# Performance work log

Measured on AMD Instinct MI355X. Metric: run time of the kernel, lower is better.

## Reference

```python
import jax, jax.numpy as jnp
import numpy as np

N_ITERS = 100   # fixed ADMM (OSQP-style) iteration count
RHO = 1.0       # ADMM penalty
SIGMA = 1e-6    # OSQP regularization


def setup_inputs() -> dict:
    key = jax.random.key(0)
    ks = jax.random.split(key, 12)
    B, S, H, nA = 16384, 512, 1024, 24
    mEq, mIneq = 4, 8
    state = jax.random.normal(ks[0], (B, S), dtype=jnp.float32)
    Aeq = jax.random.normal(ks[1], (mEq, nA), dtype=jnp.float32)
    beq = jax.random.normal(ks[2], (mEq,), dtype=jnp.float32)
    A = jax.random.normal(ks[3], (mIneq, nA), dtype=jnp.float32)
    b = jax.random.uniform(ks[4], (mIneq,), dtype=jnp.float32)
    ub = jnp.ones((nA,), dtype=jnp.float32)
    lb = jnp.zeros((nA,), dtype=jnp.float32)
    # MLP parameters (3 Dense layers as in the flax module)
    W1 = jax.random.normal(ks[5], (S, H), dtype=jnp.float32) / np.sqrt(S).astype(np.float32)
    b1 = jnp.zeros((H,), dtype=jnp.float32)
    W2 = jax.random.normal(ks[6], (H, H), dtype=jnp.float32) / np.sqrt(H).astype(np.float32)
    b2 = jnp.zeros((H,), dtype=jnp.float32)
    W3 = jax.random.normal(ks[7], (H, nA), dtype=jnp.float32) / np.sqrt(H).astype(np.float32)
    b3 = jnp.zeros((nA,), dtype=jnp.float32)
    return dict(state=state, Aeq=Aeq, beq=beq, A=A, b=b, ub=ub, lb=lb,
                W1=W1, b1=b1, W2=W2, b2=b2, W3=W3, b3=b3)


def reference(state, Aeq, beq, A, b, ub, lb, W1, b1, W2, b2, W3, b3):
    # ---- 3-layer MLP ----
    h = jax.nn.relu(state @ W1 + b1)
    h = jax.nn.relu(h @ W2 + b2)
    raw = h @ W3 + b3                      # [B, n]
    n = raw.shape[-1]
    I = jnp.eye(n, dtype=raw.dtype)
    # ---- stack constraints exactly as solve_qp: [Aeq; A_ineq; I; -I] ----
    A_tot = jnp.concatenate([Aeq, A, I, -I], axis=0)            # [M, n]
    neg_inf = jnp.full((A.shape[0],), -jnp.inf, dtype=raw.dtype)
    l_tot = jnp.concatenate([beq, neg_inf, lb, -ub])            # [M]
    u_tot = jnp.concatenate([beq, b, ub, -lb])                  # [M]
    # ---- OSQP-style ADMM: min 0.5||x||^2 - raw'x  s.t. l <= A_tot x <= u ----
    q = -raw                                                    # [B, n]
    M = (1.0 + SIGMA) * I + RHO * (A_tot.T @ A_tot)             # [n, n] (P = I)
    Minv = jnp.linalg.inv(M)
    B_, m = q.shape[0], A_tot.shape[0]
    X0 = jnp.zeros_like(q)
    Z0 = jnp.zeros((B_, m), dtype=q.dtype)
    Y0 = jnp.zeros((B_, m), dtype=q.dtype)

    def step(carry, _):
        X, Z, Y = carry
        rhs = SIGMA * X - q + (RHO * Z - Y) @ A_tot             # [B, n]
        Xn = rhs @ Minv.T                                       # [B, n]
        Zt = Xn @ A_tot.T                                       # [B, m]
        Zn = jnp.clip(Zt + Y / RHO, l_tot, u_tot)
        Yn = Y + RHO * (Zt - Zn)
        return (Xn, Zn, Yn), None

    (X, Z, Y), _ = jax.lax.scan(step, (X0, Z0, Y0), None, length=N_ITERS)
    return X
```

## Files before the change

kernel.cpp:

```cpp
#include <hip/hip_runtime.h>

using uint = unsigned int;
using ushort = unsigned short;

typedef __attribute__((ext_vector_type(8))) short bf16x8;
typedef __attribute__((ext_vector_type(4))) short bf16x4;
typedef __attribute__((ext_vector_type(4))) float f32x4;

#define ADMM_ITERS 100
#define RHO_C 1.0f
#define SIGMA_C 1e-6f

__device__ inline ushort f2bf(float f) {
  union { float f; uint u; } c; c.f = f;
  uint u = c.u;
  uint r = (u + 0x7fffu + ((u >> 16) & 1u)) >> 16;
  return (ushort)r;
}

__device__ inline void gload_lds16(const void* g, void* l) {
  __builtin_amdgcn_global_load_lds(
      (const __attribute__((address_space(1))) void*)g,
      (__attribute__((address_space(3))) void*)l, 16, 0, 0);
}

__device__ inline void splitPack(const float* x, bf16x8& hi, bf16x8& lo) {
#pragma unroll
  for (int j = 0; j < 8; ++j) {
    uint b = __float_as_uint(x[j]);
    uint hb = b & 0xffff0000u;
    float lf = x[j] - __uint_as_float(hb);
    hi[j] = (short)(b >> 16);
    lo[j] = (short)(__float_as_uint(lf) >> 16);
  }
}

__device__ inline void splitPack4(const f32x4& x, bf16x4& hi, bf16x4& lo) {
  uint b0 = __float_as_uint(x[0]), b1 = __float_as_uint(x[1]);
  uint b2 = __float_as_uint(x[2]), b3 = __float_as_uint(x[3]);
  float l0 = x[0] - __uint_as_float(b0 & 0xffff0000u);
  float l1 = x[1] - __uint_as_float(b1 & 0xffff0000u);
  float l2 = x[2] - __uint_as_float(b2 & 0xffff0000u);
  float l3 = x[3] - __uint_as_float(b3 & 0xffff0000u);
  union { uint u[2]; bf16x4 v; } ch, cl;
  ch.u[0] = __builtin_amdgcn_perm(b1, b0, 0x07060302u);
  ch.u[1] = __builtin_amdgcn_perm(b3, b2, 0x07060302u);
  cl.u[0] = __builtin_amdgcn_perm(__float_as_uint(l1), __float_as_uint(l0), 0x07060302u);
  cl.u[1] = __builtin_amdgcn_perm(__float_as_uint(l3), __float_as_uint(l2), 0x07060302u);
  hi = ch.v; lo = cl.v;
}

__device__ void transpose_body(const float* __restrict__ in, ushort* __restrict__ out,
                               int R, int C, int Cout, int bx, int by, int tid) {
  __shared__ float t[32][33];
  const int c0 = bx * 32, r0 = by * 32;
  const int tx = tid & 31, ty = tid >> 5;
  for (int rr = ty; rr < 32; rr += 8) {
    int r = r0 + rr, c = c0 + tx;
    float v = 0.0f;
    if (r < R && c < C) v = in[(long)r * C + c];
    t[rr][tx] = v;
  }
  __syncthreads();
  for (int rr = ty; rr < 32; rr += 8) {
    int c = c0 + rr, r = r0 + tx;
    if (c < Cout && r < R) out[(long)c * R + r] = f2bf(t[tx][rr]);
  }
}

__device__ void setup_body(const float* __restrict__ Aeq, const float* __restrict__ beq,
                           const float* __restrict__ A, const float* __restrict__ b,
                           const float* __restrict__ ub, const float* __restrict__ lb,
                           ushort* __restrict__ Th, ushort* __restrict__ Tl,
                           ushort* __restrict__ T0h, ushort* __restrict__ T0l,
                           float* __restrict__ blp, float* __restrict__ bup, int t) {
  __shared__ float Aug[24][48];
  __shared__ float A12[12 * 24];
  __shared__ float fac[24];
  __shared__ float Tx[24][36];
  for (int i = t; i < 48 * 64; i += 256) { Th[i] = 0; Tl[i] = 0; }
  for (int i = t; i < 48 * 32; i += 256) { T0h[i] = 0; T0l[i] = 0; }
  if (t < 96)  A12[t] = Aeq[t];
  if (t < 192) A12[96 + t] = A[t];
  __syncthreads();
  for (int idx = t; idx < 576; idx += 256) {
    int j = idx / 24, k = idx % 24;
    float s = (j == k) ? (1.0f + SIGMA_C + 2.0f * RHO_C) : 0.0f;
    for (int r = 0; r < 12; ++r) s += RHO_C * A12[r * 24 + j] * A12[r * 24 + k];
    Aug[j][k] = s;
    Aug[j][24 + k] = (j == k) ? 1.0f : 0.0f;
  }
  __syncthreads();
  for (int p = 0; p < 24; ++p) {
    float rp = 1.0f / Aug[p][p];
    if (t < 24) fac[t] = Aug[t][p];
    __syncthreads();
    if (t < 48) Aug[p][t] *= rp;
    __syncthreads();
    for (int idx = t; idx < 24 * 48; idx += 256) {
      int r = idx / 48, c = idx % 48;
      if (r != p) Aug[r][c] -= fac[r] * Aug[p][c];
    }
    __syncthreads();
  }
  auto splitStore = [](ushort* hp, ushort* lp, int i, float v) {
    ushort hs = f2bf(v);
    float hf = __uint_as_float(((uint)hs) << 16);
    ushort ls = f2bf(v - hf);
    hp[i] = hs; lp[i] = ls;
  };
  for (int idx = t; idx < 24 * 36; idx += 256) {
    int n = idx / 36, k = idx % 36;
    float v;
    if (k < 24) v = 2.0f * Aug[n][24 + k];
    else {
      v = 0.0f;
      for (int j = 0; j < 24; ++j) v += Aug[n][24 + j] * A12[(k - 24) * 24 + j];
    }
    Tx[n][k] = v;
    splitStore(Th, Tl, n * 64 + k, v);
  }
  __syncthreads();
  for (int idx = t; idx < 12 * 36; idx += 256) {
    int m = idx / 36, k = idx % 36;
    float v = 0.0f;
    for (int j = 0; j < 24; ++j) v += A12[m * 24 + j] * Tx[j][k];
    splitStore(Th, Tl, (24 + m) * 64 + k, v);
  }
  for (int idx = t; idx < 36 * 24; idx += 256) {
    int n = idx / 24, k = idx % 24;
    float v;
    if (n < 24) v = Aug[n][24 + k];
    else {
      v = 0.0f;
      for (int j = 0; j < 24; ++j) v += A12[(n - 24) * 24 + j] * Aug[j][24 + k];
    }
    splitStore(T0h, T0l, n * 32 + k, v);
  }
  if (t < 48) {
    float lv, uv;
    if (t < 24)      { lv = lb[t]; uv = ub[t]; }
    else if (t < 28) { lv = beq[t - 24]; uv = lv; }
    else if (t < 36) { lv = -1e30f; uv = b[t - 28]; }
    else             { lv = -1e30f; uv = 1e30f; }
    blp[t] = lv; bup[t] = uv;
  }
}

__global__ void prep_all(
    const float* __restrict__ state, ushort* __restrict__ stateB, int n4,
    const float* __restrict__ W1, ushort* __restrict__ W1T,
    const float* __restrict__ W2, ushort* __restrict__ W2T,
    const float* __restrict__ W3, ushort* __restrict__ W3T,
    const float* __restrict__ Aeq, const float* __restrict__ beq,
    const float* __restrict__ A, const float* __restrict__ b,
    const float* __restrict__ ub, const float* __restrict__ lb,
    ushort* __restrict__ Th, ushort* __restrict__ Tl,
    ushort* __restrict__ T0h, ushort* __restrict__ T0l,
    float* __restrict__ blp, float* __restrict__ bup) {
  const int nConv = n4 >> 8;
  int bb = blockIdx.x;
  if (bb < nConv) {
    int i = bb * 256 + threadIdx.x;
    if (i < n4) {
      float4 v = ((const float4*)state)[i];
      uint2 p;
      p.x = (uint)f2bf(v.x) | ((uint)f2bf(v.y) << 16);
      p.y = (uint)f2bf(v.z) | ((uint)f2bf(v.w) << 16);
      ((uint2*)stateB)[i] = p;
    }
    return;
  }
  bb -= nConv;
  if (bb < 512)  { transpose_body(W1, W1T, 512, 1024, 1024, bb & 31, bb >> 5, threadIdx.x); return; }
  bb -= 512;
  if (bb < 1024) { transpose_body(W2, W2T, 1024, 1024, 1024, bb & 31, bb >> 5, threadIdx.x); return; }
  bb -= 1024;
  if (bb < 32)   { transpose_body(W3, W3T, 1024, 24, 32, 0, bb, threadIdx.x); return; }
  setup_body(Aeq, beq, A, b, ub, lb, Th, Tl, T0h, T0l, blp, bup, threadIdx.x);
}

template<int BM, int BN, int WM, int WN, int TM, int TN, int MODE>
__global__ __launch_bounds__(256) void gemm_bt(
    const ushort* __restrict__ A, const ushort* __restrict__ Bt,
    const float* __restrict__ bias, void* __restrict__ Cout_,
    int K, int ldc, int nvalid) {
  __shared__ char lds[(BM + BN) * 64];
  char* ldsA = lds;
  char* ldsB = lds + BM * 64;

  const int tid = threadIdx.x;
  const int wave = tid >> 6;
  const int lane = tid & 63;
  const int blockM = blockIdx.y * BM;
  const int blockN = blockIdx.x * BN;
  const int wm = (wave / WN) * (TM * 16);
  const int wn = (wave % WN) * (TN * 16);

  f32x4 acc[TM][TN] = {};

  const int l15 = lane & 15;
  const int kq = lane >> 4;
  constexpr int AI = BM / 16;
  constexpr int TOT = (BM + BN) / 16;
  const int srow = lane >> 2;
  const int kb = (lane & 3) ^ ((srow >> 1) & 3);

  for (int k0 = 0; k0 < K; k0 += 32) {
    for (int inst = wave; inst < TOT; inst += 4) {
      const bool isA = inst < AI;
      const int i = isA ? inst : inst - AI;
      const ushort* gp = (isA ? A : Bt)
          + (long)((isA ? blockM : blockN) + i * 16 + srow) * K + (k0 + kb * 8);
      char* lp = (isA ? ldsA : ldsB) + i * 1024;
      gload_lds16(gp, lp);
    }
    __syncthreads();

    bf16x8 af[TM], bfr[TN];
#pragma unroll
    for (int i = 0; i < TM; ++i) {
      int r = wm + i * 16 + l15;
      int ch = kq ^ ((r >> 1) & 3);
      af[i] = *(const bf16x8*)(ldsA + r * 64 + ch * 16);
    }
#pragma unroll
    for (int j = 0; j < TN; ++j) {
      int r = wn + j * 16 + l15;
      int ch = kq ^ ((r >> 1) & 3);
      bfr[j] = *(const bf16x8*)(ldsB + r * 64 + ch * 16);
    }
#pragma unroll
    for (int i = 0; i < TM; ++i)
#pragma unroll
      for (int j = 0; j < TN; ++j)
        acc[i][j] = __builtin_amdgcn_mfma_f32_16x16x32_bf16(af[i], bfr[j], acc[i][j], 0, 0, 0);
    __syncthreads();
  }

  const int ro = lane >> 4;
#pragma unroll
  for (int i = 0; i < TM; ++i) {
#pragma unroll
    for (int j = 0; j < TN; ++j) {
      const int col = blockN + wn + j * 16 + l15;
      float bv;
      if (MODE == 0) bv = bias[col];
      else bv = (col < nvalid) ? bias[col] : 0.0f;
#pragma unroll
      for (int r = 0; r < 4; ++r) {
        const int row = blockM + wm + i * 16 + ro * 4 + r;
        float v = acc[i][j][r] + bv;
        if (MODE == 0) {
          v = fmaxf(v, 0.0f);
          ((ushort*)Cout_)[(long)row * ldc + col] = f2bf(v);
        } else {
          if (col < nvalid) ((float*)Cout_)[(long)row * ldc + col] = v;
        }
      }
    }
  }
}

#define GEMM8P_QUAD(MI0, NJ0)                                                 \
  _Pragma("unroll") for (int mi_ = 0; mi_ < 4; ++mi_)                         \
  _Pragma("unroll") for (int nj_ = 0; nj_ < 2; ++nj_)                         \
  _Pragma("unroll") for (int kk_ = 0; kk_ < 2; ++kk_)                         \
    acc[(MI0) + mi_][(NJ0) + nj_] = __builtin_amdgcn_mfma_f32_16x16x32_bf16(  \
        aF[mi_][kk_], bF[(NJ0) + nj_][kk_], acc[(MI0) + mi_][(NJ0) + nj_],    \
        0, 0, 0);

#define GEMM8P_SYNC_PRE()                              \
  __builtin_amdgcn_s_barrier();                        \
  asm volatile("s_waitcnt lgkmcnt(0)" ::: "memory");   \
  __builtin_amdgcn_sched_barrier(0);                   \
  __builtin_amdgcn_s_setprio(1);

#define GEMM8P_SYNC_POST()                             \
  __builtin_amdgcn_s_setprio(0);                       \
  __builtin_amdgcn_s_barrier();

__global__ __launch_bounds__(512, 2) void gemm8p(
    const ushort* __restrict__ A, const ushort* __restrict__ Bt,
    const float* __restrict__ bias, ushort* __restrict__ Cout,
    int K, int ldc, int nblk_n) {
  __shared__ __align__(16) char ldsc[131072];

  const int nwg = gridDim.x;
  const int bid = blockIdx.x;
  const int swz = (bid & 7) * (nwg >> 3) + (bid >> 3);
  const int blockM = (swz / nblk_n) * 256;
  const int blockN = (swz % nblk_n) * 256;

  const int tid = threadIdx.x;
  const int wave = tid >> 6;
  const int lane = tid & 63;
  const int l15 = lane & 15;
  const int q = lane >> 4;
  const int wm = (wave >> 2) * 128;
  const int wn = (wave & 3) * 64;
  const int nt = K >> 6;

  f32x4 acc[8][4] = {};

  auto stage = [&](int ts, int h) {
    if (ts >= nt) return;
    char* base = ldsc + ((ts & 1) << 16) + (h << 14);
#pragma unroll
    for (int j = 0; j < 2; ++j) {
      const int idx = wave * 64 + j * 512 + lane;
      const int row = idx >> 3;
      const int cs = (idx & 7) ^ (row & 7);
      const ushort* gp =
          (h < 2 ? A + (long)(blockM + ((h & 1) << 7) + row) * K
                 : Bt + (long)(blockN + ((h & 1) << 7) + row) * K)
          + (ts << 6) + cs * 8;
      gload_lds16(gp, base + ((wave * 64 + j * 512) << 4));
    }
  };
  auto dsA = [&](int cb, int mi, int kk) {
    const int r = wm + mi * 16 + l15;
    const int cs = (kk * 4 + q) ^ (r & 7);
    return *(const bf16x8*)(ldsc + (cb << 16) + r * 128 + cs * 16);
  };
  auto dsB = [&](int cb, int nj, int kk) {
    const int r = wn + nj * 16 + l15;
    const int cs = (kk * 4 + q) ^ (r & 7);
    return *(const bf16x8*)(ldsc + (cb << 16) + 32768 + r * 128 + cs * 16);
  };

  stage(0, 0); stage(0, 1); stage(0, 2); stage(0, 3);
  stage(1, 0);
  asm volatile("s_waitcnt vmcnt(2)" ::: "memory");
  __builtin_amdgcn_s_barrier();

  bf16x8 aF[4][2], bF[4][2];
#pragma unroll 1
  for (int t = 0; t < nt; ++t) {
    const int cb = t & 1;
#pragma unroll
    for (int mi = 0; mi < 4; ++mi)
#pragma unroll
      for (int kk = 0; kk < 2; ++kk) aF[mi][kk] = dsA(cb, mi, kk);
#pragma unroll
    for (int nj = 0; nj < 2; ++nj)
#pragma unroll
      for (int kk = 0; kk < 2; ++kk) bF[nj][kk] = dsB(cb, nj, kk);
    stage(t + 1, 1);
    GEMM8P_SYNC_PRE();
    GEMM8P_QUAD(0, 0);
    GEMM8P_SYNC_POST();
#pragma unroll
    for (int nj = 2; nj < 4; ++nj)
#pragma unroll
      for (int kk = 0; kk < 2; ++kk) bF[nj][kk] = dsB(cb, nj, kk);
    stage(t + 1, 2);
    GEMM8P_SYNC_PRE();
    GEMM8P_QUAD(0, 2);
    GEMM8P_SYNC_POST();
#pragma unroll
    for (int mi = 0; mi < 4; ++mi)
#pragma unroll
      for (int kk = 0; kk < 2; ++kk) aF[mi][kk] = dsA(cb, 4 + mi, kk);
    stage(t + 1, 3);
    GEMM8P_SYNC_PRE();
    GEMM8P_QUAD(4, 2);
    GEMM8P_SYNC_POST();
    stage(t + 2, 0);
    if (t + 2 < nt) { asm volatile("s_waitcnt vmcnt(2)" ::: "memory"); }
    else            { asm volatile("s_waitcnt vmcnt(0)" ::: "memory"); }
    __builtin_amdgcn_s_barrier();
    __builtin_amdgcn_s_setprio(1);
    GEMM8P_QUAD(4, 0);
    GEMM8P_SYNC_POST();
  }

#pragma unroll
  for (int mi = 0; mi < 8; ++mi) {
#pragma unroll
    for (int nj = 0; nj < 4; ++nj) {
      const int col = blockN + wn + nj * 16 + l15;
      const float bv = bias[col];
#pragma unroll
      for (int r = 0; r < 4; ++r) {
        const int row = blockM + wm + mi * 16 + q * 4 + r;
        float v = acc[mi][nj][r] + bv;
        v = fmaxf(v, 0.0f);
        Cout[(long)row * ldc + col] = f2bf(v);
      }
    }
  }
}

#define MFMA16(a, b, c) __builtin_amdgcn_mfma_f32_16x16x16bf16_1k(a, b, c, 0, 0, 0)

__global__ __launch_bounds__(256, 1) void admm_mfma(
    const float* __restrict__ raw,
    const ushort* __restrict__ Th, const ushort* __restrict__ Tl,
    const ushort* __restrict__ T0h, const ushort* __restrict__ T0l,
    const float* __restrict__ blp, const float* __restrict__ bup,
    float* __restrict__ outp) {
  const int tid = threadIdx.x, wave = tid >> 6, lane = tid & 63;
  const int l15 = lane & 15, q = lane >> 4;
  const long rowbase = (long)blockIdx.x * 64 + wave * 16;

  f32x4 bl[3], bu[3];
#pragma unroll
  for (int t = 0; t < 3; ++t) {
    bl[t] = *(const f32x4*)(blp + 16 * t + 4 * q);
    bu[t] = *(const f32x4*)(bup + 16 * t + 4 * q);
  }

  f32x4 W[3], base[3];
  {
    bf16x8 t0h[3], t0l[3];
#pragma unroll
    for (int t = 0; t < 3; ++t) {
      t0h[t] = *(const bf16x8*)(T0h + (16 * t + l15) * 32 + q * 8);
      t0l[t] = *(const bf16x8*)(T0l + (16 * t + l15) * 32 + q * 8);
    }
    float qa[8];
    if (q < 3) {
      const float* rp = raw + (rowbase + l15) * 24 + q * 8;
      float4 v0 = *(const float4*)rp;
      float4 v1 = *(const float4*)(rp + 4);
      qa[0] = v0.x; qa[1] = v0.y; qa[2] = v0.z; qa[3] = v0.w;
      qa[4] = v1.x; qa[5] = v1.y; qa[6] = v1.z; qa[7] = v1.w;
    } else {
#pragma unroll
      for (int j = 0; j < 8; ++j) qa[j] = 0.0f;
    }
    bf16x8 qhi, qlo;
    splitPack(qa, qhi, qlo);
#pragma unroll
    for (int t = 0; t < 3; ++t) {
      f32x4 acc = {0.0f, 0.0f, 0.0f, 0.0f};
      acc = __builtin_amdgcn_mfma_f32_16x16x32_bf16(t0h[t], qhi, acc, 0, 0, 0);
      acc = __builtin_amdgcn_mfma_f32_16x16x32_bf16(t0h[t], qlo, acc, 0, 0, 0);
      acc = __builtin_amdgcn_mfma_f32_16x16x32_bf16(t0l[t], qhi, acc, 0, 0, 0);
      base[t] = acc; W[t] = acc;
    }
  }

  bf16x4 th[3][3], tl[3][3];
#pragma unroll
  for (int t = 0; t < 3; ++t)
#pragma unroll
    for (int c = 0; c < 3; ++c) {
      th[t][c] = *(const bf16x4*)(Th + (16 * t + l15) * 64 + 16 * c + 4 * q);
      tl[t][c] = *(const bf16x4*)(Tl + (16 * t + l15) * 64 + 16 * c + 4 * q);
    }

  f32x4 y01[2];
#pragma unroll 1
  for (int it = 1; it < ADMM_ITERS; ++it) {
    bf16x4 uh[3], ul[3];
    f32x4 C[3];
#pragma unroll
    for (int t = 0; t < 3; ++t) {
      f32x4 u;
#pragma unroll
      for (int r = 0; r < 4; ++r) {
        float w = W[t][r];
        float z = fminf(fmaxf(w, bl[t][r]), bu[t][r]);
        float yy = w - z;
        u[r] = z - yy;
        C[t][r] = base[t][r] + yy;
        if (t < 2) y01[t][r] = yy;
      }
      splitPack4(u, uh[t], ul[t]);
    }
#pragma unroll
    for (int t = 0; t < 3; ++t) {
      f32x4 a0 = C[t];
      f32x4 a1 = {0.0f, 0.0f, 0.0f, 0.0f};
      f32x4 a2 = {0.0f, 0.0f, 0.0f, 0.0f};
      a0 = MFMA16(th[t][0], uh[0], a0);
      a0 = MFMA16(th[t][0], ul[0], a0);
      a0 = MFMA16(tl[t][0], uh[0], a0);
      a1 = MFMA16(th[t][1], uh[1], a1);
      a1 = MFMA16(th[t][1], ul[1], a1);
      a1 = MFMA16(tl[t][1], uh[1], a1);
      a2 = MFMA16(th[t][2], uh[2], a2);
      a2 = MFMA16(th[t][2], ul[2], a2);
      a2 = MFMA16(tl[t][2], uh[2], a2);
      W[t] = (a0 + a1) + a2;
    }
  }

#pragma unroll
  for (int t = 0; t < 2; ++t) {
    if (t == 0 || q < 2) {
      f32x4 x;
#pragma unroll
      for (int r = 0; r < 4; ++r) x[r] = W[t][r] - y01[t][r];
      *(f32x4*)(outp + (rowbase + l15) * 24 + 16 * t + 4 * q) = x;
    }
  }
}

extern "C" void kernel_launch(void* const* d_in, const int* in_sizes, int n_in,
                              void* d_out, int out_size, void* d_ws, size_t ws_size,
                              hipStream_t stream) {
  const float* state = (const float*)d_in[0];
  const float* Aeq   = (const float*)d_in[1];
  const float* beq   = (const float*)d_in[2];
  const float* Ain   = (const float*)d_in[3];
  const float* bin   = (const float*)d_in[4];
  const float* ub    = (const float*)d_in[5];
  const float* lb    = (const float*)d_in[6];
  const float* W1    = (const float*)d_in[7];
  const float* b1    = (const float*)d_in[8];
  const float* W2    = (const float*)d_in[9];
  const float* b2    = (const float*)d_in[10];
  const float* W3    = (const float*)d_in[11];
  const float* b3    = (const float*)d_in[12];

  const int Bn = in_sizes[0] / 512;
  char* ws = (char*)d_ws;
  ushort* stateB = (ushort*)(ws + 0);
  ushort* W1T    = (ushort*)(ws + 16777216);
  ushort* W2T    = (ushort*)(ws + 17825792);
  ushort* W3T    = (ushort*)(ws + 19922944);
  ushort* Th     = (ushort*)(ws + 19993600);
  ushort* Tl     = (ushort*)(ws + 19999744);
  ushort* T0h    = (ushort*)(ws + 20005888);
  ushort* T0l    = (ushort*)(ws + 20008960);
  float*  blp    = (float*) (ws + 20012032);
  float*  bup    = (float*) (ws + 20012224);
  ushort* H1     = (ushort*)(ws + 21565440);
  ushort* H2     = (ushort*)(ws + 55119872);
  float*  rawb   = (float*)d_out;

  const int n4 = (Bn * 512) / 4;
  const int nConv = n4 / 256;
  const int nPrep = nConv + 512 + 1024 + 32 + 1;
  prep_all<<<nPrep, 256, 0, stream>>>(state, stateB, n4, W1, W1T, W2, W2T, W3, W3T,
                                      Aeq, beq, Ain, bin, ub, lb,
                                      Th, Tl, T0h, T0l, blp, bup);

  const int nblkN = 1024 / 256;
  const int nwg = (Bn / 256) * nblkN;
  gemm8p<<<nwg, 512, 0, stream>>>(stateB, W1T, b1, H1, 512, 1024, nblkN);
  gemm8p<<<nwg, 512, 0, stream>>>(H1, W2T, b2, H2, 1024, 1024, nblkN);
  gemm_bt<64, 32, 4, 1, 1, 2, 1><<<dim3(1, Bn / 64), 256, 0, stream>>>(
      H2, W3T, b3, rawb, 1024, 24, 24);

  admm_mfma<<<Bn / 64, 256, 0, stream>>>(rawb, Th, Tl, T0h, T0l, blp, bup,
                                         (float*)d_out);
}
```

Before: 256.4 us.

## Interleave ADMM pack and MFMA chains, peel final iteration, relax launch bounds

Restructures the ADMM inner loop so the MFMAs for each constraint block start as soon as that block's clip-and-split is packed, instead of after all three packs. Accumulations are reordered to run three independent output tiles side by side, giving more MFMA-level parallelism. The last iteration is peeled and computes only the two output tiles, writing X straight from the MFMA result. This removes the kept y01 state and the final subtraction. Dropping the min-blocks hint from launch_bounds lets the compiler pick register allocation more freely, which may change occupancy.

```diff
diff --git a/kernel.cpp b/kernel.cpp
--- a/kernel.cpp
+++ b/kernel.cpp
@@ -394,7 +394,7 @@
 
 #define MFMA16(a, b, c) __builtin_amdgcn_mfma_f32_16x16x16bf16_1k(a, b, c, 0, 0, 0)
 
-__global__ __launch_bounds__(256, 1) void admm_mfma(
+__global__ __launch_bounds__(256) void admm_mfma(
     const float* __restrict__ raw,
     const ushort* __restrict__ Th, const ushort* __restrict__ Tl,
     const ushort* __restrict__ T0h, const ushort* __restrict__ T0l,
@@ -451,52 +451,96 @@
       tl[t][c] = *(const bf16x4*)(Tl + (16 * t + l15) * 64 + 16 * c + 4 * q);
     }
 
-  f32x4 y01[2];
+#define PACKT(t, UH, UL, CC)                                         \
+  {                                                                  \
+    f32x4 u_;                                                        \
+    _Pragma("unroll") for (int r = 0; r < 4; ++r) {                  \
+      float w_ = W[t][r];                                            \
+      float z_ = fminf(fmaxf(w_, bl[t][r]), bu[t][r]);               \
+      float yy_ = w_ - z_;                                           \
+      u_[r] = z_ - yy_;                                              \
+      CC[r] = base[t][r] + yy_;                                      \
+    }                                                                \
+    splitPack4(u_, UH, UL);                                          \
+  }
+
+  const f32x4 z4 = {0.0f, 0.0f, 0.0f, 0.0f};
+
 #pragma unroll 1
-  for (int it = 1; it < ADMM_ITERS; ++it) {
-    bf16x4 uh[3], ul[3];
-    f32x4 C[3];
-#pragma unroll
-    for (int t = 0; t < 3; ++t) {
-      f32x4 u;
-#pragma unroll
-      for (int r = 0; r < 4; ++r) {
-        float w = W[t][r];
-        float z = fminf(fmaxf(w, bl[t][r]), bu[t][r]);
-        float yy = w - z;
-        u[r] = z - yy;
-        C[t][r] = base[t][r] + yy;
-        if (t < 2) y01[t][r] = yy;
-      }
-      splitPack4(u, uh[t], ul[t]);
-    }
-#pragma unroll
-    for (int t = 0; t < 3; ++t) {
-      f32x4 a0 = C[t];
-      f32x4 a1 = {0.0f, 0.0f, 0.0f, 0.0f};
-      f32x4 a2 = {0.0f, 0.0f, 0.0f, 0.0f};
-      a0 = MFMA16(th[t][0], uh[0], a0);
-      a0 = MFMA16(th[t][0], ul[0], a0);
-      a0 = MFMA16(tl[t][0], uh[0], a0);
-      a1 = MFMA16(th[t][1], uh[1], a1);
-      a1 = MFMA16(th[t][1], ul[1], a1);
-      a1 = MFMA16(tl[t][1], uh[1], a1);
-      a2 = MFMA16(th[t][2], uh[2], a2);
-      a2 = MFMA16(th[t][2], ul[2], a2);
-      a2 = MFMA16(tl[t][2], uh[2], a2);
-      W[t] = (a0 + a1) + a2;
-    }
-  }
-
-#pragma unroll
-  for (int t = 0; t < 2; ++t) {
-    if (t == 0 || q < 2) {
-      f32x4 x;
-#pragma unroll
-      for (int r = 0; r < 4; ++r) x[r] = W[t][r] - y01[t][r];
-      *(f32x4*)(outp + (rowbase + l15) * 24 + 16 * t + 4 * q) = x;
-    }
-  }
+  for (int it = 2; it < ADMM_ITERS; ++it) {
+    bf16x4 uh0, ul0, uh1, ul1, uh2, ul2;
+    f32x4 C0, C1, C2;
+    f32x4 a00, a10, a20, a01, a11, a21, a02, a12, a22;
+
+    PACKT(0, uh0, ul0, C0);
+    a00 = MFMA16(th[0][0], uh0, z4);
+    a10 = MFMA16(th[1][0], uh0, z4);
+    a20 = MFMA16(th[2][0], uh0, z4);
+    a00 = MFMA16(th[0][0], ul0, a00);
+    a10 = MFMA16(th[1][0], ul0, a10);
+    a20 = MFMA16(th[2][0], ul0, a20);
+    a00 = MFMA16(tl[0][0], uh0, a00);
+    a10 = MFMA16(tl[1][0], uh0, a10);
+    a20 = MFMA16(tl[2][0], uh0, a20);
+
+    PACKT(1, uh1, ul1, C1);
+    a01 = MFMA16(th[0][1], uh1, z4);
+    a11 = MFMA16(th[1][1], uh1, z4);
+    a21 = MFMA16(th[2][1], uh1, z4);
+    a01 = MFMA16(th[0][1], ul1, a01);
+    a11 = MFMA16(th[1][1], ul1, a11);
+    a21 = MFMA16(th[2][1], ul1, a21);
+    a01 = MFMA16(tl[0][1], uh1, a01);
+    a11 = MFMA16(tl[1][1], uh1, a11);
+    a21 = MFMA16(tl[2][1], uh1, a21);
+
+    PACKT(2, uh2, ul2, C2);
+    a02 = MFMA16(th[0][2], uh2, C0);
+    a12 = MFMA16(th[1][2], uh2, C1);
+    a22 = MFMA16(th[2][2], uh2, C2);
+    a02 = MFMA16(th[0][2], ul2, a02);
+    a12 = MFMA16(th[1][2], ul2, a12);
+    a22 = MFMA16(th[2][2], ul2, a22);
+    a02 = MFMA16(tl[0][2], uh2, a02);
+    a12 = MFMA16(tl[1][2], uh2, a12);
+    a22 = MFMA16(tl[2][2], uh2, a22);
+
+    W[0] = (a00 + a01) + a02;
+    W[1] = (a10 + a11) + a12;
+    W[2] = (a20 + a21) + a22;
+  }
+
+  {
+    bf16x4 uh0, ul0, uh1, ul1, uh2, ul2;
+    f32x4 C0, C1, C2;
+    PACKT(0, uh0, ul0, C0);
+    PACKT(1, uh1, ul1, C1);
+    PACKT(2, uh2, ul2, C2);
+    f32x4 x00, x10, x01, x11, x02, x12;
+    x00 = MFMA16(th[0][0], uh0, z4);
+    x10 = MFMA16(th[1][0], uh0, z4);
+    x00 = MFMA16(th[0][0], ul0, x00);
+    x10 = MFMA16(th[1][0], ul0, x10);
+    x00 = MFMA16(tl[0][0], uh0, x00);
+    x10 = MFMA16(tl[1][0], uh0, x10);
+    x01 = MFMA16(th[0][1], uh1, z4);
+    x11 = MFMA16(th[1][1], uh1, z4);
+    x01 = MFMA16(th[0][1], ul1, x01);
+    x11 = MFMA16(th[1][1], ul1, x11);
+    x01 = MFMA16(tl[0][1], uh1, x01);
+    x11 = MFMA16(tl[1][1], uh1, x11);
+    x02 = MFMA16(th[0][2], uh2, base[0]);
+    x12 = MFMA16(th[1][2], uh2, base[1]);
+    x02 = MFMA16(th[0][2], ul2, x02);
+    x12 = MFMA16(th[1][2], ul2, x12);
+    x02 = MFMA16(tl[0][2], uh2, x02);
+    x12 = MFMA16(tl[1][2], uh2, x12);
+    f32x4 X0 = (x00 + x01) + x02;
+    f32x4 X1 = (x10 + x11) + x12;
+    *(f32x4*)(outp + (rowbase + l15) * 24 + 4 * q) = X0;
+    if (q < 2) *(f32x4*)(outp + (rowbase + l15) * 24 + 16 + 4 * q) = X1;
+  }
+#undef PACKT
 }
 
 extern "C" void kernel_launch(void* const* d_in, const int* in_sizes, int n_in,
```

Result: faster. 250.7 us (-2.2%).

## Restage ADMM iterate through LDS to use wider-K MFMA with fewer instructions

Applied to the files above, without the earlier changes.

The ADMM kernel now splits each iterate into hi/lo bf16 pairs and writes them to a swizzled per-wave LDS buffer. It reads them back in the operand layout of the 16x16x32 MFMA, so each iteration issues 18 wider-K MFMAs instead of 27 narrower ones, with the three output tiles interleaved for independent accumulation chains. The last iteration is peeled and computes only the two output tiles needed, dropping the stored dual term. The launch grows to 512 blocks, where the extra 256 redo the same rows and skip the store, likely to fill occupancy. That adds redundant work and LDS traffic in exchange for fewer matrix instructions.

```diff
diff --git a/kernel.cpp b/kernel.cpp
--- a/kernel.cpp
+++ b/kernel.cpp
@@ -35,19 +35,18 @@
   }
 }
 
-__device__ inline void splitPack4(const f32x4& x, bf16x4& hi, bf16x4& lo) {
+__device__ inline void packPairs(const f32x4& x, uint& h0, uint& h1,
+                                 uint& l0, uint& l1) {
   uint b0 = __float_as_uint(x[0]), b1 = __float_as_uint(x[1]);
   uint b2 = __float_as_uint(x[2]), b3 = __float_as_uint(x[3]);
-  float l0 = x[0] - __uint_as_float(b0 & 0xffff0000u);
-  float l1 = x[1] - __uint_as_float(b1 & 0xffff0000u);
-  float l2 = x[2] - __uint_as_float(b2 & 0xffff0000u);
-  float l3 = x[3] - __uint_as_float(b3 & 0xffff0000u);
-  union { uint u[2]; bf16x4 v; } ch, cl;
-  ch.u[0] = __builtin_amdgcn_perm(b1, b0, 0x07060302u);
-  ch.u[1] = __builtin_amdgcn_perm(b3, b2, 0x07060302u);
-  cl.u[0] = __builtin_amdgcn_perm(__float_as_uint(l1), __float_as_uint(l0), 0x07060302u);
-  cl.u[1] = __builtin_amdgcn_perm(__float_as_uint(l3), __float_as_uint(l2), 0x07060302u);
-  hi = ch.v; lo = cl.v;
+  float r0 = x[0] - __uint_as_float(b0 & 0xffff0000u);
+  float r1 = x[1] - __uint_as_float(b1 & 0xffff0000u);
+  float r2 = x[2] - __uint_as_float(b2 & 0xffff0000u);
+  float r3 = x[3] - __uint_as_float(b3 & 0xffff0000u);
+  h0 = __builtin_amdgcn_perm(b1, b0, 0x07060302u);
+  h1 = __builtin_amdgcn_perm(b3, b2, 0x07060302u);
+  l0 = __builtin_amdgcn_perm(__float_as_uint(r1), __float_as_uint(r0), 0x07060302u);
+  l1 = __builtin_amdgcn_perm(__float_as_uint(r3), __float_as_uint(r2), 0x07060302u);
 }
 
 __device__ void transpose_body(const float* __restrict__ in, ushort* __restrict__ out,
@@ -392,17 +391,29 @@
   }
 }
 
-#define MFMA16(a, b, c) __builtin_amdgcn_mfma_f32_16x16x16bf16_1k(a, b, c, 0, 0, 0)
-
-__global__ __launch_bounds__(256, 1) void admm_mfma(
+__global__ __launch_bounds__(256) void admm_mfma(
     const float* __restrict__ raw,
     const ushort* __restrict__ Th, const ushort* __restrict__ Tl,
     const ushort* __restrict__ T0h, const ushort* __restrict__ T0l,
     const float* __restrict__ blp, const float* __restrict__ bup,
     float* __restrict__ outp) {
+  __shared__ __align__(16) float UL[4][1152];
   const int tid = threadIdx.x, wave = tid >> 6, lane = tid & 63;
   const int l15 = lane & 15, q = lane >> 4;
-  const long rowbase = (long)blockIdx.x * 64 + wave * 16;
+  const int bid = blockIdx.x;
+  const bool dowrite = bid < 256;
+  const long rowbase = (long)(bid & 255) * 64 + wave * 16;
+
+  float* ubase = UL[wave];
+  for (int i = lane; i < 1152; i += 64) ubase[i] = 0.0f;
+
+  const int l7 = l15 & 7;
+  uint* uw = (uint*)ubase;
+  uint* wp0 = uw + 36 * l15 + (((0 + (q >> 1)) ^ l7) << 2) + 2 * (q & 1);
+  uint* wp1 = uw + 36 * l15 + (((2 + (q >> 1)) ^ l7) << 2) + 2 * (q & 1);
+  uint* wp2 = uw + 36 * l15 + (((4 + (q >> 1)) ^ l7) << 2) + 2 * (q & 1);
+  const float* rp0 = ubase + 36 * l15 + ((q ^ l7) << 2);
+  const float* rp1 = ubase + 36 * l15 + (((4 + q) ^ l7) << 2);
 
   f32x4 bl[3], bu[3];
 #pragma unroll
@@ -442,61 +453,90 @@
     }
   }
 
-  bf16x4 th[3][3], tl[3][3];
+  bf16x8 th[3][2], tl[3][2];
 #pragma unroll
   for (int t = 0; t < 3; ++t)
 #pragma unroll
-    for (int c = 0; c < 3; ++c) {
-      th[t][c] = *(const bf16x4*)(Th + (16 * t + l15) * 64 + 16 * c + 4 * q);
-      tl[t][c] = *(const bf16x4*)(Tl + (16 * t + l15) * 64 + 16 * c + 4 * q);
-    }
-
-  f32x4 y01[2];
+    for (int c = 0; c < 2; ++c) {
+      th[t][c] = *(const bf16x8*)(Th + (16 * t + l15) * 64 + 32 * c + q * 8);
+      tl[t][c] = *(const bf16x8*)(Tl + (16 * t + l15) * 64 + 32 * c + q * 8);
+    }
+
+#define PACKST(t, WPT, CC)                                           \
+  {                                                                  \
+    f32x4 u_;                                                        \
+    _Pragma("unroll") for (int r = 0; r < 4; ++r) {                  \
+      float w_ = W[t][r];                                            \
+      float z_ = fminf(fmaxf(w_, bl[t][r]), bu[t][r]);               \
+      float yy_ = w_ - z_;                                           \
+      u_[r] = z_ - yy_;                                              \
+      CC[r] = base[t][r] + yy_;                                      \
+    }                                                                \
+    uint h0_, h1_, l0_, l1_;                                         \
+    packPairs(u_, h0_, h1_, l0_, l1_);                               \
+    WPT[0] = h0_; WPT[1] = h1_; WPT[576] = l0_; WPT[577] = l1_;      \
+  }
+
 #pragma unroll 1
-  for (int it = 1; it < ADMM_ITERS; ++it) {
-    bf16x4 uh[3], ul[3];
-    f32x4 C[3];
-#pragma unroll
-    for (int t = 0; t < 3; ++t) {
-      f32x4 u;
-#pragma unroll
-      for (int r = 0; r < 4; ++r) {
-        float w = W[t][r];
-        float z = fminf(fmaxf(w, bl[t][r]), bu[t][r]);
-        float yy = w - z;
-        u[r] = z - yy;
-        C[t][r] = base[t][r] + yy;
-        if (t < 2) y01[t][r] = yy;
-      }
-      splitPack4(u, uh[t], ul[t]);
-    }
-#pragma unroll
-    for (int t = 0; t < 3; ++t) {
-      f32x4 a0 = C[t];
-      f32x4 a1 = {0.0f, 0.0f, 0.0f, 0.0f};
-      f32x4 a2 = {0.0f, 0.0f, 0.0f, 0.0f};
-      a0 = MFMA16(th[t][0], uh[0], a0);
-      a0 = MFMA16(th[t][0], ul[0], a0);
-      a0 = MFMA16(tl[t][0], uh[0], a0);
-      a1 = MFMA16(th[t][1], uh[1], a1);
-      a1 = MFMA16(th[t][1], ul[1], a1);
-      a1 = MFMA16(tl[t][1], uh[1], a1);
-      a2 = MFMA16(th[t][2], uh[2], a2);
-      a2 = MFMA16(th[t][2], ul[2], a2);
-      a2 = MFMA16(tl[t][2], uh[2], a2);
-      W[t] = (a0 + a1) + a2;
-    }
-  }
-
-#pragma unroll
-  for (int t = 0; t < 2; ++t) {
-    if (t == 0 || q < 2) {
-      f32x4 x;
-#pragma unroll
-      for (int r = 0; r < 4; ++r) x[r] = W[t][r] - y01[t][r];
-      *(f32x4*)(outp + (rowbase + l15) * 24 + 16 * t + 4 * q) = x;
-    }
-  }
+  for (int it = 2; it < ADMM_ITERS; ++it) {
+    f32x4 C0, C1, C2;
+    PACKST(0, wp0, C0);
+    PACKST(1, wp1, C1);
+    PACKST(2, wp2, C2);
+    bf16x8 uh0 = *(const bf16x8*)rp0;
+    bf16x8 uh1 = *(const bf16x8*)rp1;
+    bf16x8 ul0 = *(const bf16x8*)(rp0 + 576);
+    bf16x8 ul1 = *(const bf16x8*)(rp1 + 576);
+    f32x4 a0 = C0, a1 = C1, a2 = C2;
+    a0 = __builtin_amdgcn_mfma_f32_16x16x32_bf16(th[0][0], uh0, a0, 0, 0, 0);
+    a1 = __builtin_amdgcn_mfma_f32_16x16x32_bf16(th[1][0], uh0, a1, 0, 0, 0);
+    a2 = __builtin_amdgcn_mfma_f32_16x16x32_bf16(th[2][0], uh0, a2, 0, 0, 0);
+    a0 = __builtin_amdgcn_mfma_f32_16x16x32_bf16(th[0][1], uh1, a0, 0, 0, 0);
+    a1 = __builtin_amdgcn_mfma_f32_16x16x32_bf16(th[1][1], uh1, a1, 0, 0, 0);
+    a2 = __builtin_amdgcn_mfma_f32_16x16x32_bf16(th[2][1], uh1, a2, 0, 0, 0);
+    a0 = __builtin_amdgcn_mfma_f32_16x16x32_bf16(th[0][0], ul0, a0, 0, 0, 0);
+    a1 = __builtin_amdgcn_mfma_f32_16x16x32_bf16(th[1][0], ul0, a1, 0, 0, 0);
+    a2 = __builtin_amdgcn_mfma_f32_16x16x32_bf16(th[2][0], ul0, a2, 0, 0, 0);
+    a0 = __builtin_amdgcn_mfma_f32_16x16x32_bf16(th[0][1], ul1, a0, 0, 0, 0);
+    a1 = __builtin_amdgcn_mfma_f32_16x16x32_bf16(th[1][1], ul1, a1, 0, 0, 0);
+    a2 = __builtin_amdgcn_mfma_f32_16x16x32_bf16(th[2][1], ul1, a2, 0, 0, 0);
+    a0 = __builtin_amdgcn_mfma_f32_16x16x32_bf16(tl[0][0], uh0, a0, 0, 0, 0);
+    a1 = __builtin_amdgcn_mfma_f32_16x16x32_bf16(tl[1][0], uh0, a1, 0, 0, 0);
+    a2 = __builtin_amdgcn_mfma_f32_16x16x32_bf16(tl[2][0], uh0, a2, 0, 0, 0);
+    a0 = __builtin_amdgcn_mfma_f32_16x16x32_bf16(tl[0][1], uh1, a0, 0, 0, 0);
+    a1 = __builtin_amdgcn_mfma_f32_16x16x32_bf16(tl[1][1], uh1, a1, 0, 0, 0);
+    a2 = __builtin_amdgcn_mfma_f32_16x16x32_bf16(tl[2][1], uh1, a2, 0, 0, 0);
+    W[0] = a0; W[1] = a1; W[2] = a2;
+  }
+
+  {
+    f32x4 C0, C1, C2;
+    PACKST(0, wp0, C0);
+    PACKST(1, wp1, C1);
+    PACKST(2, wp2, C2);
+    bf16x8 uh0 = *(const bf16x8*)rp0;
+    bf16x8 uh1 = *(const bf16x8*)rp1;
+    bf16x8 ul0 = *(const bf16x8*)(rp0 + 576);
+    bf16x8 ul1 = *(const bf16x8*)(rp1 + 576);
+    f32x4 x0 = base[0], x1 = base[1];
+    x0 = __builtin_amdgcn_mfma_f32_16x16x32_bf16(th[0][0], uh0, x0, 0, 0, 0);
+    x1 = __builtin_amdgcn_mfma_f32_16x16x32_bf16(th[1][0], uh0, x1, 0, 0, 0);
+    x0 = __builtin_amdgcn_mfma_f32_16x16x32_bf16(th[0][1], uh1, x0, 0, 0, 0);
+    x1 = __builtin_amdgcn_mfma_f32_16x16x32_bf16(th[1][1], uh1, x1, 0, 0, 0);
+    x0 = __builtin_amdgcn_mfma_f32_16x16x32_bf16(th[0][0], ul0, x0, 0, 0, 0);
+    x1 = __builtin_amdgcn_mfma_f32_16x16x32_bf16(th[1][0], ul0, x1, 0, 0, 0);
+    x0 = __builtin_amdgcn_mfma_f32_16x16x32_bf16(th[0][1], ul1, x0, 0, 0, 0);
+    x1 = __builtin_amdgcn_mfma_f32_16x16x32_bf16(th[1][1], ul1, x1, 0, 0, 0);
+    x0 = __builtin_amdgcn_mfma_f32_16x16x32_bf16(tl[0][0], uh0, x0, 0, 0, 0);
+    x1 = __builtin_amdgcn_mfma_f32_16x16x32_bf16(tl[1][0], uh0, x1, 0, 0, 0);
+    x0 = __builtin_amdgcn_mfma_f32_16x16x32_bf16(tl[0][1], uh1, x0, 0, 0, 0);
+    x1 = __builtin_amdgcn_mfma_f32_16x16x32_bf16(tl[1][1], uh1, x1, 0, 0, 0);
+    if (dowrite) {
+      *(f32x4*)(outp + (rowbase + l15) * 24 + 4 * q) = x0;
+      if (q < 2) *(f32x4*)(outp + (rowbase + l15) * 24 + 16 + 4 * q) = x1;
+    }
+  }
+#undef PACKST
 }
 
 extern "C" void kernel_launch(void* const* d_in, const int* in_sizes, int n_in,
@@ -546,6 +586,6 @@
   gemm_bt<64, 32, 4, 1, 1, 2, 1><<<dim3(1, Bn / 64), 256, 0, stream>>>(
       H2, W3T, b3, rawb, 1024, 24, 24);
 
-  admm_mfma<<<Bn / 64, 256, 0, stream>>>(rawb, Th, Tl, T0h, T0l, blp, bup,
-                                         (float*)d_out);
-}
+  admm_mfma<<<512, 256, 0, stream>>>(rawb, Th, Tl, T0h, T0l, blp, bup,
+                                     (float*)d_out);
+}
```

Result: slower. 287.8 us (+12.2%).

## Split ADMM state tiles across three waves with LDS exchange per iteration

Applied to the files above, without the earlier changes.

The ADMM kernel now handles 16 batch rows per block with three waves, one per 16-wide output tile, rather than one wave computing all three tiles for its 16 rows. Each iteration a wave packs its clipped update into double-buffered LDS, synchronises, reads the full update vector, and runs six K=32 MFMAs in place of nine K=16 ones. The goal is more wave-level parallelism across CUs and a shorter per-wave dependency chain on this latency-bound loop. In exchange every iteration pays an LDS round trip and a block barrier, and the loop start and final-step handling are restructured.

```diff
diff --git a/kernel.cpp b/kernel.cpp
--- a/kernel.cpp
+++ b/kernel.cpp
@@ -35,19 +35,18 @@
   }
 }
 
-__device__ inline void splitPack4(const f32x4& x, bf16x4& hi, bf16x4& lo) {
+__device__ inline void packPairs(const f32x4& x, uint& h0, uint& h1,
+                                 uint& l0, uint& l1) {
   uint b0 = __float_as_uint(x[0]), b1 = __float_as_uint(x[1]);
   uint b2 = __float_as_uint(x[2]), b3 = __float_as_uint(x[3]);
-  float l0 = x[0] - __uint_as_float(b0 & 0xffff0000u);
-  float l1 = x[1] - __uint_as_float(b1 & 0xffff0000u);
-  float l2 = x[2] - __uint_as_float(b2 & 0xffff0000u);
-  float l3 = x[3] - __uint_as_float(b3 & 0xffff0000u);
-  union { uint u[2]; bf16x4 v; } ch, cl;
-  ch.u[0] = __builtin_amdgcn_perm(b1, b0, 0x07060302u);
-  ch.u[1] = __builtin_amdgcn_perm(b3, b2, 0x07060302u);
-  cl.u[0] = __builtin_amdgcn_perm(__float_as_uint(l1), __float_as_uint(l0), 0x07060302u);
-  cl.u[1] = __builtin_amdgcn_perm(__float_as_uint(l3), __float_as_uint(l2), 0x07060302u);
-  hi = ch.v; lo = cl.v;
+  float r0 = x[0] - __uint_as_float(b0 & 0xffff0000u);
+  float r1 = x[1] - __uint_as_float(b1 & 0xffff0000u);
+  float r2 = x[2] - __uint_as_float(b2 & 0xffff0000u);
+  float r3 = x[3] - __uint_as_float(b3 & 0xffff0000u);
+  h0 = __builtin_amdgcn_perm(b1, b0, 0x07060302u);
+  h1 = __builtin_amdgcn_perm(b3, b2, 0x07060302u);
+  l0 = __builtin_amdgcn_perm(__float_as_uint(r1), __float_as_uint(r0), 0x07060302u);
+  l1 = __builtin_amdgcn_perm(__float_as_uint(r3), __float_as_uint(r2), 0x07060302u);
 }
 
 __device__ void transpose_body(const float* __restrict__ in, ushort* __restrict__ out,
@@ -392,33 +391,30 @@
   }
 }
 
-#define MFMA16(a, b, c) __builtin_amdgcn_mfma_f32_16x16x16bf16_1k(a, b, c, 0, 0, 0)
-
-__global__ __launch_bounds__(256, 1) void admm_mfma(
+__global__ __launch_bounds__(192) void admm_mfma(
     const float* __restrict__ raw,
     const ushort* __restrict__ Th, const ushort* __restrict__ Tl,
     const ushort* __restrict__ T0h, const ushort* __restrict__ T0l,
     const float* __restrict__ blp, const float* __restrict__ bup,
     float* __restrict__ outp) {
-  const int tid = threadIdx.x, wave = tid >> 6, lane = tid & 63;
+  __shared__ __align__(16) float U2[2 * 1152];
+  const int tid = threadIdx.x, wv = tid >> 6, lane = tid & 63;
   const int l15 = lane & 15, q = lane >> 4;
-  const long rowbase = (long)blockIdx.x * 64 + wave * 16;
-
-  f32x4 bl[3], bu[3];
-#pragma unroll
-  for (int t = 0; t < 3; ++t) {
-    bl[t] = *(const f32x4*)(blp + 16 * t + 4 * q);
-    bu[t] = *(const f32x4*)(bup + 16 * t + 4 * q);
-  }
-
-  f32x4 W[3], base[3];
+  const long rowbase = (long)blockIdx.x * 16;
+
+  for (int i = tid; i < 2304; i += 192) U2[i] = 0.0f;
+
+  uint* uw = (uint*)U2;
+  const int wofs = 36 * l15 + 2 * q + 8 * wv;
+  const int rofs = 36 * l15 + 4 * q;
+
+  const f32x4 bl = *(const f32x4*)(blp + 16 * wv + 4 * q);
+  const f32x4 bu = *(const f32x4*)(bup + 16 * wv + 4 * q);
+
+  f32x4 W, base;
   {
-    bf16x8 t0h[3], t0l[3];
-#pragma unroll
-    for (int t = 0; t < 3; ++t) {
-      t0h[t] = *(const bf16x8*)(T0h + (16 * t + l15) * 32 + q * 8);
-      t0l[t] = *(const bf16x8*)(T0l + (16 * t + l15) * 32 + q * 8);
-    }
+    bf16x8 t0h = *(const bf16x8*)(T0h + (16 * wv + l15) * 32 + q * 8);
+    bf16x8 t0l = *(const bf16x8*)(T0l + (16 * wv + l15) * 32 + q * 8);
     float qa[8];
     if (q < 3) {
       const float* rp = raw + (rowbase + l15) * 24 + q * 8;
@@ -432,69 +428,87 @@
     }
     bf16x8 qhi, qlo;
     splitPack(qa, qhi, qlo);
-#pragma unroll
-    for (int t = 0; t < 3; ++t) {
-      f32x4 acc = {0.0f, 0.0f, 0.0f, 0.0f};
-      acc = __builtin_amdgcn_mfma_f32_16x16x32_bf16(t0h[t], qhi, acc, 0, 0, 0);
-      acc = __builtin_amdgcn_mfma_f32_16x16x32_bf16(t0h[t], qlo, acc, 0, 0, 0);
-      acc = __builtin_amdgcn_mfma_f32_16x16x32_bf16(t0l[t], qhi, acc, 0, 0, 0);
-      base[t] = acc; W[t] = acc;
-    }
-  }
-
-  bf16x4 th[3][3], tl[3][3];
-#pragma unroll
-  for (int t = 0; t < 3; ++t)
-#pragma unroll
-    for (int c = 0; c < 3; ++c) {
-      th[t][c] = *(const bf16x4*)(Th + (16 * t + l15) * 64 + 16 * c + 4 * q);
-      tl[t][c] = *(const bf16x4*)(Tl + (16 * t + l15) * 64 + 16 * c + 4 * q);
-    }
-
-  f32x4 y01[2];
+    f32x4 acc = {0.0f, 0.0f, 0.0f, 0.0f};
+    acc = __builtin_amdgcn_mfma_f32_16x16x32_bf16(t0h, qhi, acc, 0, 0, 0);
+    acc = __builtin_amdgcn_mfma_f32_16x16x32_bf16(t0h, qlo, acc, 0, 0, 0);
+    acc = __builtin_amdgcn_mfma_f32_16x16x32_bf16(t0l, qhi, acc, 0, 0, 0);
+    base = acc; W = acc;
+  }
+
+  const bf16x8 th0 = *(const bf16x8*)(Th + (16 * wv + l15) * 64 + q * 8);
+  const bf16x8 th1 = *(const bf16x8*)(Th + (16 * wv + l15) * 64 + 32 + q * 8);
+  const bf16x8 tl0 = *(const bf16x8*)(Tl + (16 * wv + l15) * 64 + q * 8);
+  const bf16x8 tl1 = *(const bf16x8*)(Tl + (16 * wv + l15) * 64 + 32 + q * 8);
+
+  __syncthreads();
+
+  const f32x4 z4 = {0.0f, 0.0f, 0.0f, 0.0f};
+
 #pragma unroll 1
-  for (int it = 1; it < ADMM_ITERS; ++it) {
-    bf16x4 uh[3], ul[3];
-    f32x4 C[3];
-#pragma unroll
-    for (int t = 0; t < 3; ++t) {
-      f32x4 u;
-#pragma unroll
-      for (int r = 0; r < 4; ++r) {
-        float w = W[t][r];
-        float z = fminf(fmaxf(w, bl[t][r]), bu[t][r]);
-        float yy = w - z;
-        u[r] = z - yy;
-        C[t][r] = base[t][r] + yy;
-        if (t < 2) y01[t][r] = yy;
+  for (int it = 2; it < ADMM_ITERS; ++it) {
+    const int db = (it & 1) ? 1152 : 0;
+    f32x4 C, u_;
+#pragma unroll
+    for (int r = 0; r < 4; ++r) {
+      float w_ = W[r];
+      float z_ = fminf(fmaxf(w_, bl[r]), bu[r]);
+      float yy_ = w_ - z_;
+      u_[r] = z_ - yy_;
+      C[r] = base[r] + yy_;
+    }
+    uint h0, h1, l0, l1;
+    packPairs(u_, h0, h1, l0, l1);
+    uint* wp = uw + db + wofs;
+    wp[0] = h0; wp[1] = h1; wp[576] = l0; wp[577] = l1;
+    __syncthreads();
+    const float* rp = U2 + db + rofs;
+    bf16x8 uh0 = *(const bf16x8*)rp;
+    bf16x8 uh1 = *(const bf16x8*)(rp + 16);
+    bf16x8 ul0 = *(const bf16x8*)(rp + 576);
+    bf16x8 ul1 = *(const bf16x8*)(rp + 592);
+    f32x4 a = C, b = z4;
+    a = __builtin_amdgcn_mfma_f32_16x16x32_bf16(th0, uh0, a, 0, 0, 0);
+    b = __builtin_amdgcn_mfma_f32_16x16x32_bf16(th1, uh1, b, 0, 0, 0);
+    a = __builtin_amdgcn_mfma_f32_16x16x32_bf16(th0, ul0, a, 0, 0, 0);
+    b = __builtin_amdgcn_mfma_f32_16x16x32_bf16(th1, ul1, b, 0, 0, 0);
+    a = __builtin_amdgcn_mfma_f32_16x16x32_bf16(tl0, uh0, a, 0, 0, 0);
+    b = __builtin_amdgcn_mfma_f32_16x16x32_bf16(tl1, uh1, b, 0, 0, 0);
+    W = a + b;
+  }
+
+  {
+    const int db = (ADMM_ITERS & 1) ? 1152 : 0;
+    f32x4 u_;
+#pragma unroll
+    for (int r = 0; r < 4; ++r) {
+      float w_ = W[r];
+      float z_ = fminf(fmaxf(w_, bl[r]), bu[r]);
+      u_[r] = z_ - (w_ - z_);
+    }
+    uint h0, h1, l0, l1;
+    packPairs(u_, h0, h1, l0, l1);
+    uint* wp = uw + db + wofs;
+    wp[0] = h0; wp[1] = h1; wp[576] = l0; wp[577] = l1;
+    __syncthreads();
+    if (wv < 2) {
+      const float* rp = U2 + db + rofs;
+      bf16x8 uh0 = *(const bf16x8*)rp;
+      bf16x8 uh1 = *(const bf16x8*)(rp + 16);
+      bf16x8 ul0 = *(const bf16x8*)(rp + 576);
+      bf16x8 ul1 = *(const bf16x8*)(rp + 592);
+      f32x4 a = base, b = z4;
+      a = __builtin_amdgcn_mfma_f32_16x16x32_bf16(th0, uh0, a, 0, 0, 0);
+      b = __builtin_amdgcn_mfma_f32_16x16x32_bf16(th1, uh1, b, 0, 0, 0);
+      a = __builtin_amdgcn_mfma_f32_16x16x32_bf16(th0, ul0, a, 0, 0, 0);
+      b = __builtin_amdgcn_mfma_f32_16x16x32_bf16(th1, ul1, b, 0, 0, 0);
+      a = __builtin_amdgcn_mfma_f32_16x16x32_bf16(tl0, uh0, a, 0, 0, 0);
+      b = __builtin_amdgcn_mfma_f32_16x16x32_bf16(tl1, uh1, b, 0, 0, 0);
+      f32x4 X = a + b;
+      if (wv == 0) {
+        *(f32x4*)(outp + (rowbase + l15) * 24 + 4 * q) = X;
+      } else if (q < 2) {
+        *(f32x4*)(outp + (rowbase + l15) * 24 + 16 + 4 * q) = X;
       }
-      splitPack4(u, uh[t], ul[t]);
-    }
-#pragma unroll
-    for (int t = 0; t < 3; ++t) {
-      f32x4 a0 = C[t];
-      f32x4 a1 = {0.0f, 0.0f, 0.0f, 0.0f};
-      f32x4 a2 = {0.0f, 0.0f, 0.0f, 0.0f};
-      a0 = MFMA16(th[t][0], uh[0], a0);
-      a0 = MFMA16(th[t][0], ul[0], a0);
-      a0 = MFMA16(tl[t][0], uh[0], a0);
-      a1 = MFMA16(th[t][1], uh[1], a1);
-      a1 = MFMA16(th[t][1], ul[1], a1);
-      a1 = MFMA16(tl[t][1], uh[1], a1);
-      a2 = MFMA16(th[t][2], uh[2], a2);
-      a2 = MFMA16(th[t][2], ul[2], a2);
-      a2 = MFMA16(tl[t][2], uh[2], a2);
-      W[t] = (a0 + a1) + a2;
-    }
-  }
-
-#pragma unroll
-  for (int t = 0; t < 2; ++t) {
-    if (t == 0 || q < 2) {
-      f32x4 x;
-#pragma unroll
-      for (int r = 0; r < 4; ++r) x[r] = W[t][r] - y01[t][r];
-      *(f32x4*)(outp + (rowbase + l15) * 24 + 16 * t + 4 * q) = x;
     }
   }
 }
@@ -546,6 +560,6 @@
   gemm_bt<64, 32, 4, 1, 1, 2, 1><<<dim3(1, Bn / 64), 256, 0, stream>>>(
       H2, W3T, b3, rawb, 1024, 24, 24);
 
-  admm_mfma<<<Bn / 64, 256, 0, stream>>>(rawb, Th, Tl, T0h, T0l, blp, bup,
+  admm_mfma<<<Bn / 16, 192, 0, stream>>>(rawb, Th, Tl, T0h, T0l, blp, bup,
                                          (float*)d_out);
 }
```

Result: faster. 249.5 us (-2.7%).
